# Kernel optimization log

Measured on AMD Instinct MI355X. Metric: run time of the kernel, lower is better.

The kernel has to match this reference:

```python
import jax, jax.numpy as jnp
import numpy as np

B, P, N, E, H, KD, M = 64, 100, 1000, 512, 8, 64, 10
SQRT_E = float(np.sqrt(E))
CLIP = 10.0


def _heads(x):
    # [b, n, H*KD] -> [b, H, n, KD]
    b, n, _ = x.shape
    return x.reshape(b, n, H, KD).transpose(0, 2, 1, 3)


def setup_inputs() -> dict:
    key = jax.random.key(0)
    ks = jax.random.split(key, 20)
    f = jnp.float32
    s = 0.02  # weight init scale
    return {
        "encoded_last_node": jax.random.normal(ks[0], (B, P, E), f),
        "encoded_last_agents": jax.random.normal(ks[1], (B, P, E), f),
        "cur_dist": jax.random.uniform(ks[2], (B, P, N), f, 1e-3, 1.0),
        "ninf_mask": jnp.zeros((B, P, N), f),
        "lengths": jax.random.uniform(ks[3], (B, P, M), f),
        "max_dis": jax.random.uniform(ks[4], (B, P, 1), f),
        "remain_max_dis": jax.random.uniform(ks[5], (B, P, 1), f),
        "q_first": 0.5 * jax.random.normal(ks[6], (B, H, P, KD), f),
        "k": 0.5 * jax.random.normal(ks[7], (B, H, N, KD), f),
        "v": 0.5 * jax.random.normal(ks[8], (B, H, N, KD), f),
        "single_head_key": 0.5 * jax.random.normal(ks[9], (B, E, N), f),
        "Wq_last_w": s * jax.random.normal(ks[10], (H * KD, 2 * E + 2), f),
        "dis_emb_w": s * jax.random.normal(ks[11], (H * KD, 4), f),
        "mh_w": s * jax.random.normal(ks[12], (E, H * KD), f),
        "mh_b": s * jax.random.normal(ks[13], (E,), f),
        "dist_alpha": jnp.ones((1,), f),
        "depot_num": jax.random.randint(ks[14], (B,), 1, M + 1),
        "route_cnt": jax.random.randint(ks[15], (B, P, 1), 0, M),
        "left_city": jax.random.randint(ks[16], (B, P), 0, N + 1),
        "city_num": N,
    }


def reference(encoded_last_node, encoded_last_agents, cur_dist, ninf_mask,
              lengths, max_dis, remain_max_dis, q_first, k, v, single_head_key,
              Wq_last_w, dis_emb_w, mh_w, mh_b, dist_alpha,
              depot_num, route_cnt, left_city, city_num):
    # route_num = depot_num - 1, broadcast to route_cnt shape [B,P,1]
    route_num = jnp.broadcast_to(depot_num[:, None, None], route_cnt.shape) - 1
    g_cur = jnp.take_along_axis(lengths, route_cnt, axis=-1)    # [B,P,1]
    g_route = jnp.take_along_axis(lengths, route_num, axis=-1)  # [B,P,1]
    q_info_in = jnp.concatenate([g_cur, g_route, max_dis, remain_max_dis], axis=-1)  # [B,P,4]
    q_info = _heads(q_info_in @ dis_emb_w.T)  # [B,H,P,KD]

    frac = 1.0 - (route_cnt + 1).astype(jnp.float32) / (route_num + 1).astype(jnp.float32)
    lc = left_city[:, :, None].astype(jnp.float32) / city_num
    q_last_in = jnp.concatenate([encoded_last_node, encoded_last_agents, frac, lc], axis=-1)  # [B,P,2E+2]
    q_last = _heads(q_last_in @ Wq_last_w.T)  # [B,H,P,KD]

    q = q_first + q_last + q_info  # [B,H,P,KD]

    # masked multi-head attention (rank3 ninf mask)
    score = jnp.einsum("bhpd,bhnd->bhpn", q, k) / jnp.sqrt(jnp.float32(KD))
    score = score + ninf_mask[:, None, :, :]
    w = jax.nn.softmax(score, axis=-1)
    out = jnp.einsum("bhpn,bhnd->bhpd", w, v)
    out_concat = out.transpose(0, 2, 1, 3).reshape(out.shape[0], out.shape[2], H * KD)  # [B,P,H*KD]
    mh = out_concat @ mh_w.T + mh_b  # [B,P,E]

    # single-head distance-biased scoring
    score2 = jnp.einsum("bpe,ben->bpn", mh, single_head_key)  # [B,P,N]
    max_dist = jnp.max(cur_dist, axis=-1, keepdims=True)
    cur_dist_out = -cur_dist / max_dist
    score_clipped = CLIP * jnp.tanh(score2 / SQRT_E + dist_alpha * cur_dist_out)
    probs = jax.nn.softmax(score_clipped + ninf_mask, axis=-1)
    return probs
```

## Files before the change

### kernel.cpp

```cpp
#include <hip/hip_runtime.h>
#include <hip/hip_bf16.h>

#define BB 64
#define PP 100
#define NN 1000
#define EE 512
#define HH 8
#define KDD 64
#define MM 10
#define ROWS (BB*PP)
#define K1K 1026
#define INVSQE 0.044194173824159216f
#define CLIPV 10.0f

union F4 { float4 v; float f[4]; };

using bf16x8 = __attribute__((ext_vector_type(8))) short;
using f32x4  = __attribute__((ext_vector_type(4))) float;

__device__ inline unsigned short f2bf(float x) {
  unsigned u = __float_as_uint(x);
  u += 0x7FFFu + ((u >> 16) & 1u);
  return (unsigned short)(u >> 16);
}

__device__ inline float fast_tanh(float x) {
  float e = __expf(2.0f * x);
  return 1.0f - 2.0f / (e + 1.0f);
}

__global__ __launch_bounds__(256) void k_rowmax(const float* __restrict__ cd,
                                                float* __restrict__ rmax) {
  int row = blockIdx.x * 4 + (threadIdx.x >> 6);
  int lane = threadIdx.x & 63;
  const float* src = cd + (size_t)row * NN;
  float m = -1e30f;
  for (int i = lane; i < NN; i += 64) m = fmaxf(m, src[i]);
  #pragma unroll
  for (int off = 32; off; off >>= 1) m = fmaxf(m, __shfl_xor(m, off));
  if (lane == 0) rmax[row] = m;
}

__global__ __launch_bounds__(256) void k_qgemm(
    const float* __restrict__ eln, const float* __restrict__ ela,
    const float* __restrict__ lengths, const float* __restrict__ max_dis,
    const float* __restrict__ remain, const float* __restrict__ q_first,
    const float* __restrict__ Wq, const float* __restrict__ dis_emb,
    const int* __restrict__ depot, const int* __restrict__ route_cnt,
    const int* __restrict__ left_city, const int* __restrict__ city_num,
    float* __restrict__ qout) {
  __shared__ unsigned short Xs[64][40];
  __shared__ unsigned short Ws[64][40];
  __shared__ float info_s[64][4];
  __shared__ float fl_s[64][2];
  const int t = threadIdx.x;
  const int lane = t & 63;
  const int w = t >> 6;
  const int lr = lane & 15, lg = lane >> 4;
  const int rowBase = blockIdx.y * 64, colBase = blockIdx.x * 64;

  if (t < 64) {
    int row = rowBase + t;
    int b = row / PP;
    int rc = route_cnt[row];
    int rn = depot[b] - 1;
    info_s[t][0] = lengths[row * MM + rc];
    info_s[t][1] = lengths[row * MM + rn];
    info_s[t][2] = max_dis[row];
    info_s[t][3] = remain[row];
    fl_s[t][0] = 1.0f - (float)(rc + 1) / (float)(rn + 1);
    fl_s[t][1] = (float)left_city[row] / (float)city_num[0];
  }

  f32x4 acc[4];
  #pragma unroll
  for (int m = 0; m < 4; ++m) { acc[m][0] = 0.f; acc[m][1] = 0.f; acc[m][2] = 0.f; acc[m][3] = 0.f; }

  for (int kt = 0; kt < 32; ++kt) {
    const float* xsrc = (kt < 16) ? eln : ela;
    const int koff = (kt & 15) * 32;
    __syncthreads();
    #pragma unroll
    for (int i = 0; i < 2; ++i) {
      int s = i * 256 + t;
      int r = s >> 3, c4 = (s & 7) * 4;
      F4 xv, wv;
      xv.v = *(const float4*)&xsrc[(size_t)(rowBase + r) * 512 + koff + c4];
      wv.v = *(const float4*)&Wq[(size_t)(colBase + r) * K1K + kt * 32 + c4];
      unsigned short* xd = &Xs[r][c4];
      unsigned short* wd = &Ws[r][c4];
      xd[0] = f2bf(xv.f[0]); xd[1] = f2bf(xv.f[1]); xd[2] = f2bf(xv.f[2]); xd[3] = f2bf(xv.f[3]);
      wd[0] = f2bf(wv.f[0]); wd[1] = f2bf(wv.f[1]); wd[2] = f2bf(wv.f[2]); wd[3] = f2bf(wv.f[3]);
    }
    __syncthreads();
    bf16x8 bfr = *(bf16x8*)&Ws[w * 16 + lr][lg * 8];
    #pragma unroll
    for (int m = 0; m < 4; ++m) {
      bf16x8 af = *(bf16x8*)&Xs[m * 16 + lr][lg * 8];
      acc[m] = __builtin_amdgcn_mfma_f32_16x16x32_bf16(af, bfr, acc[m], 0, 0, 0);
    }
  }

  const int o = colBase + w * 16 + lr;
  F4 de; de.v = *(const float4*)&dis_emb[(size_t)o * 4];
  const float wq1024 = Wq[(size_t)o * K1K + 1024];
  const float wq1025 = Wq[(size_t)o * K1K + 1025];
  const int h = o >> 6, kd = o & 63;
  #pragma unroll
  for (int m = 0; m < 4; ++m) {
    #pragma unroll
    for (int j = 0; j < 4; ++j) {
      int r = m * 16 + lg * 4 + j;
      int row = rowBase + r;
      int b = row / PP, p = row % PP;
      F4 inf; inf.v = *(const float4*)&info_s[r][0];
      float v = acc[m][j]
              + inf.f[0] * de.f[0] + inf.f[1] * de.f[1]
              + inf.f[2] * de.f[2] + inf.f[3] * de.f[3]
              + fl_s[r][0] * wq1024 + fl_s[r][1] * wq1025
              + q_first[(((size_t)b * HH + h) * PP + p) * KDD + kd];
      qout[(size_t)row * 512 + o] = v;
    }
  }
}

__global__ __launch_bounds__(256) void k_attn(
    const float* __restrict__ qin, const float* __restrict__ kk,
    const float* __restrict__ vv, const float* __restrict__ mask,
    float* __restrict__ attn_out) {
  __shared__ unsigned short Kl[64][72];
  __shared__ unsigned short Vt[64][72];
  __shared__ float PM[112][68];

  const int t = threadIdx.x;
  const int lane = t & 63;
  const int w = t >> 6;
  const int lr = lane & 15;
  const int lg = lane >> 4;
  const int bh = blockIdx.x, b = bh >> 3, h = bh & 7;

  #pragma unroll
  for (int i = 0; i < 7; ++i) {
    int idx = i * 256 + t;
    int r = idx >> 4, c4 = (idx & 15) * 4;
    float4 qv = make_float4(0.f, 0.f, 0.f, 0.f);
    if (r < PP)
      qv = *(const float4*)&qin[((size_t)(b * PP + r)) * 512 + h * 64 + c4];
    qv.x *= 0.125f; qv.y *= 0.125f; qv.z *= 0.125f; qv.w *= 0.125f;
    *(float4*)&PM[r][c4] = qv;
  }
  __syncthreads();

  bf16x8 qf[2][2];
  #pragma unroll
  for (int u = 0; u < 2; ++u) {
    int tt = w + 4 * u;
    if (tt < 7) {
      #pragma unroll
      for (int kb = 0; kb < 2; ++kb) {
        F4 p0, p1;
        p0.v = *(const float4*)&PM[tt * 16 + lr][kb * 32 + lg * 8];
        p1.v = *(const float4*)&PM[tt * 16 + lr][kb * 32 + lg * 8 + 4];
        bf16x8 f;
        #pragma unroll
        for (int i = 0; i < 4; ++i) { f[i] = (short)f2bf(p0.f[i]); f[i + 4] = (short)f2bf(p1.f[i]); }
        qf[u][kb] = f;
      }
    }
  }
  __syncthreads();

  float Mx[2][4], Lx[2][4];
  f32x4 Oa[2][4];
  #pragma unroll
  for (int u = 0; u < 2; ++u)
    #pragma unroll
    for (int j = 0; j < 4; ++j) {
      Mx[u][j] = -1e30f; Lx[u][j] = 0.f;
      Oa[u][j][0] = 0.f; Oa[u][j][1] = 0.f; Oa[u][j][2] = 0.f; Oa[u][j][3] = 0.f;
    }

  for (int ch = 0; ch < 16; ++ch) {
    const int n0 = ch * 64;
    #pragma unroll
    for (int i = 0; i < 4; ++i) {
      int idx = i * 256 + t;
      int r = idx >> 4, c4 = (idx & 15) * 4;
      int n = n0 + r;
      F4 kv; kv.v = make_float4(0.f, 0.f, 0.f, 0.f);
      if (n < NN) kv.v = *(const float4*)&kk[(((size_t)bh * NN) + n) * 64 + c4];
      Kl[r][c4 + 0] = f2bf(kv.f[0]); Kl[r][c4 + 1] = f2bf(kv.f[1]);
      Kl[r][c4 + 2] = f2bf(kv.f[2]); Kl[r][c4 + 3] = f2bf(kv.f[3]);
    }
    {
      int a = t >> 4, b2 = t & 15;
      F4 rowv[4];
      #pragma unroll
      for (int r = 0; r < 4; ++r) {
        int n = n0 + 4 * a + r;
        rowv[r].v = (n < NN) ? *(const float4*)&vv[(((size_t)bh * NN) + n) * 64 + 4 * b2]
                             : make_float4(0.f, 0.f, 0.f, 0.f);
      }
      #pragma unroll
      for (int c = 0; c < 4; ++c) {
        unsigned short* dst = &Vt[4 * b2 + c][4 * a];
        dst[0] = f2bf(rowv[0].f[c]); dst[1] = f2bf(rowv[1].f[c]);
        dst[2] = f2bf(rowv[2].f[c]); dst[3] = f2bf(rowv[3].f[c]);
      }
    }
    #pragma unroll
    for (int i = 0; i < 7; ++i) {
      int idx = i * 256 + t;
      int r = idx >> 4, c4 = (idx & 15) * 4;
      int n = n0 + c4;
      F4 mv; mv.v = make_float4(0.f, 0.f, 0.f, 0.f);
      if (r < PP) {
        if (n + 3 < NN) {
          mv.v = *(const float4*)&mask[((size_t)(b * PP + r)) * NN + n];
        } else {
          #pragma unroll
          for (int j = 0; j < 4; ++j)
            mv.f[j] = (n + j < NN) ? mask[((size_t)(b * PP + r)) * NN + n + j] : -1e30f;
        }
      }
      *(float4*)&PM[r][c4] = mv.v;
    }
    __syncthreads();

    float rsv[2][4];
    #pragma unroll
    for (int u = 0; u < 2; ++u) {
      int tt = w + 4 * u;
      if (tt >= 7) continue;
      f32x4 sa[4];
      #pragma unroll
      for (int nb = 0; nb < 4; ++nb) { sa[nb][0] = 0.f; sa[nb][1] = 0.f; sa[nb][2] = 0.f; sa[nb][3] = 0.f; }
      #pragma unroll
      for (int kb = 0; kb < 2; ++kb)
        #pragma unroll
        for (int nb = 0; nb < 4; ++nb) {
          bf16x8 kf = *(bf16x8*)&Kl[nb * 16 + lr][kb * 32 + lg * 8];
          sa[nb] = __builtin_amdgcn_mfma_f32_16x16x32_bf16(qf[u][kb], kf, sa[nb], 0, 0, 0);
        }
      #pragma unroll
      for (int j = 0; j < 4; ++j) {
        int pl = tt * 16 + lg * 4 + j;
        float s0 = sa[0][j] + PM[pl][lr];
        float s1 = sa[1][j] + PM[pl][16 + lr];
        float s2 = sa[2][j] + PM[pl][32 + lr];
        float s3 = sa[3][j] + PM[pl][48 + lr];
        float cm = fmaxf(fmaxf(s0, s1), fmaxf(s2, s3));
        #pragma unroll
        for (int off = 1; off < 16; off <<= 1) cm = fmaxf(cm, __shfl_xor(cm, off));
        float Mn = fmaxf(Mx[u][j], cm);
        float r = __expf(Mx[u][j] - Mn);
        float e0 = __expf(s0 - Mn), e1 = __expf(s1 - Mn);
        float e2 = __expf(s2 - Mn), e3 = __expf(s3 - Mn);
        float sum = (e0 + e1) + (e2 + e3);
        #pragma unroll
        for (int off = 1; off < 16; off <<= 1) sum += __shfl_xor(sum, off);
        Lx[u][j] = Lx[u][j] * r + sum;
        Mx[u][j] = Mn;
        rsv[u][j] = r;
        PM[pl][lr] = e0; PM[pl][16 + lr] = e1; PM[pl][32 + lr] = e2; PM[pl][48 + lr] = e3;
      }
    }
    __syncthreads();

    #pragma unroll
    for (int u = 0; u < 2; ++u) {
      int tt = w + 4 * u;
      if (tt >= 7) continue;
      #pragma unroll
      for (int dt = 0; dt < 4; ++dt) {
        f32x4 o = Oa[u][dt];
        o[0] *= rsv[u][0]; o[1] *= rsv[u][1]; o[2] *= rsv[u][2]; o[3] *= rsv[u][3];
        Oa[u][dt] = o;
      }
      #pragma unroll
      for (int kb = 0; kb < 2; ++kb) {
        F4 p0, p1;
        p0.v = *(const float4*)&PM[tt * 16 + lr][kb * 32 + lg * 8];
        p1.v = *(const float4*)&PM[tt * 16 + lr][kb * 32 + lg * 8 + 4];
        bf16x8 pf;
        #pragma unroll
        for (int i = 0; i < 4; ++i) { pf[i] = (short)f2bf(p0.f[i]); pf[i + 4] = (short)f2bf(p1.f[i]); }
        #pragma unroll
        for (int dt = 0; dt < 4; ++dt) {
          bf16x8 vf = *(bf16x8*)&Vt[dt * 16 + lr][kb * 32 + lg * 8];
          Oa[u][dt] = __builtin_amdgcn_mfma_f32_16x16x32_bf16(pf, vf, Oa[u][dt], 0, 0, 0);
        }
      }
    }
    __syncthreads();
  }

  #pragma unroll
  for (int u = 0; u < 2; ++u) {
    int tt = w + 4 * u;
    if (tt >= 7) continue;
    #pragma unroll
    for (int j = 0; j < 4; ++j) {
      int p = tt * 16 + lg * 4 + j;
      if (p >= PP) continue;
      float L = Lx[u][j];
      float inv = (L > 0.f) ? 1.0f / L : 0.f;
      #pragma unroll
      for (int dt = 0; dt < 4; ++dt)
        attn_out[((size_t)(b * PP + p)) * 512 + h * 64 + dt * 16 + lr] = Oa[u][dt][j] * inv;
    }
  }
}

__global__ __launch_bounds__(256) void k_mhgemm(
    const float* __restrict__ A, const float* __restrict__ W,
    const float* __restrict__ bias, float* __restrict__ out) {
  __shared__ unsigned short Xs[64][40];
  __shared__ unsigned short Ws[64][40];
  const int t = threadIdx.x;
  const int lane = t & 63;
  const int w = t >> 6;
  const int lr = lane & 15, lg = lane >> 4;
  const int rowBase = blockIdx.y * 64, colBase = blockIdx.x * 64;

  f32x4 acc[4];
  #pragma unroll
  for (int m = 0; m < 4; ++m) { acc[m][0] = 0.f; acc[m][1] = 0.f; acc[m][2] = 0.f; acc[m][3] = 0.f; }

  for (int kt = 0; kt < 16; ++kt) {
    const int koff = kt * 32;
    __syncthreads();
    #pragma unroll
    for (int i = 0; i < 2; ++i) {
      int s = i * 256 + t;
      int r = s >> 3, c4 = (s & 7) * 4;
      F4 xv, wv;
      xv.v = *(const float4*)&A[(size_t)(rowBase + r) * 512 + koff + c4];
      wv.v = *(const float4*)&W[(size_t)(colBase + r) * 512 + koff + c4];
      unsigned short* xd = &Xs[r][c4];
      unsigned short* wd = &Ws[r][c4];
      xd[0] = f2bf(xv.f[0]); xd[1] = f2bf(xv.f[1]); xd[2] = f2bf(xv.f[2]); xd[3] = f2bf(xv.f[3]);
      wd[0] = f2bf(wv.f[0]); wd[1] = f2bf(wv.f[1]); wd[2] = f2bf(wv.f[2]); wd[3] = f2bf(wv.f[3]);
    }
    __syncthreads();
    bf16x8 bfr = *(bf16x8*)&Ws[w * 16 + lr][lg * 8];
    #pragma unroll
    for (int m = 0; m < 4; ++m) {
      bf16x8 af = *(bf16x8*)&Xs[m * 16 + lr][lg * 8];
      acc[m] = __builtin_amdgcn_mfma_f32_16x16x32_bf16(af, bfr, acc[m], 0, 0, 0);
    }
  }

  const int o = colBase + w * 16 + lr;
  const float bv = bias[o];
  #pragma unroll
  for (int m = 0; m < 4; ++m) {
    #pragma unroll
    for (int j = 0; j < 4; ++j) {
      int row = rowBase + m * 16 + lg * 4 + j;
      out[(size_t)row * 512 + o] = acc[m][j] + bv;
    }
  }
}

__global__ __launch_bounds__(256) void k_final_score(
    const float* __restrict__ mh, const float* __restrict__ shk,
    const float* __restrict__ cur_dist, const float* __restrict__ rmax,
    const float* __restrict__ mask, const float* __restrict__ dist_alpha,
    float* __restrict__ sc_out) {
  __shared__ unsigned short As[112][40];
  __shared__ unsigned short Bt[64][40];
  const int t = threadIdx.x;
  const int lane = t & 63;
  const int w = t >> 6;
  const int lr = lane & 15, lg = lane >> 4;
  const int n0 = blockIdx.x * 64, b = blockIdx.y;

  f32x4 acc[7];
  #pragma unroll
  for (int m = 0; m < 7; ++m) { acc[m][0] = 0.f; acc[m][1] = 0.f; acc[m][2] = 0.f; acc[m][3] = 0.f; }

  for (int kt = 0; kt < 16; ++kt) {
    const int k0 = kt * 32;
    __syncthreads();
    #pragma unroll
    for (int i = 0; i < 4; ++i) {
      int s = i * 256 + t;
      if (s < 896) {
        int r = s >> 3, c4 = (s & 7) * 4;
        F4 xv; xv.v = make_float4(0.f, 0.f, 0.f, 0.f);
        if (r < PP) xv.v = *(const float4*)&mh[(size_t)(b * PP + r) * 512 + k0 + c4];
        unsigned short* xd = &As[r][c4];
        xd[0] = f2bf(xv.f[0]); xd[1] = f2bf(xv.f[1]); xd[2] = f2bf(xv.f[2]); xd[3] = f2bf(xv.f[3]);
      }
    }
    if (t < 128) {
      int a = t & 15, kb = t >> 4;
      F4 rowv[4];
      #pragma unroll
      for (int r = 0; r < 4; ++r) {
        int k = k0 + 4 * kb + r;
        int n = n0 + 4 * a;
        rowv[r].v = (n < NN) ? *(const float4*)&shk[((size_t)b * EE + k) * NN + n]
                             : make_float4(0.f, 0.f, 0.f, 0.f);
      }
      #pragma unroll
      for (int c = 0; c < 4; ++c) {
        unsigned short* dst = &Bt[4 * a + c][4 * kb];
        dst[0] = f2bf(rowv[0].f[c]); dst[1] = f2bf(rowv[1].f[c]);
        dst[2] = f2bf(rowv[2].f[c]); dst[3] = f2bf(rowv[3].f[c]);
      }
    }
    __syncthreads();
    bf16x8 bfr = *(bf16x8*)&Bt[w * 16 + lr][lg * 8];
    #pragma unroll
    for (int m = 0; m < 7; ++m) {
      bf16x8 af = *(bf16x8*)&As[m * 16 + lr][lg * 8];
      acc[m] = __builtin_amdgcn_mfma_f32_16x16x32_bf16(af, bfr, acc[m], 0, 0, 0);
    }
  }

  const float alpha = dist_alpha[0];
  const int n = n0 + w * 16 + lr;
  if (n < NN) {
    #pragma unroll
    for (int m = 0; m < 7; ++m) {
      #pragma unroll
      for (int j = 0; j < 4; ++j) {
        int p = m * 16 + lg * 4 + j;
        if (p >= PP) continue;
        size_t rb = (size_t)(b * PP + p) * NN;
        float rmx = rmax[b * PP + p];
        float cd = cur_dist[rb + n];
        float mk = mask[rb + n];
        sc_out[rb + n] = CLIPV * fast_tanh(acc[m][j] * INVSQE - alpha * cd / rmx) + mk;
      }
    }
  }
}

__global__ __launch_bounds__(256) void k_softmax(const float* __restrict__ sc,
                                                 float* __restrict__ out) {
  __shared__ float redm[4];
  __shared__ float redsum[4];
  const int row = blockIdx.x;
  const int t = threadIdx.x;
  const float* src = sc + (size_t)row * NN;
  float v0[4];
  float m = -1e30f;
  #pragma unroll
  for (int i = 0; i < 4; ++i) {
    int n = i * 256 + t;
    v0[i] = (n < NN) ? src[n] : -1e30f;
    m = fmaxf(m, v0[i]);
  }
  #pragma unroll
  for (int off = 32; off; off >>= 1) m = fmaxf(m, __shfl_xor(m, off));
  int wid = t >> 6, lane = t & 63;
  if (lane == 0) redm[wid] = m;
  __syncthreads();
  m = fmaxf(fmaxf(redm[0], redm[1]), fmaxf(redm[2], redm[3]));
  float e[4];
  float s = 0.f;
  #pragma unroll
  for (int i = 0; i < 4; ++i) {
    int n = i * 256 + t;
    e[i] = (n < NN) ? __expf(v0[i] - m) : 0.f;
    s += e[i];
  }
  #pragma unroll
  for (int off = 32; off; off >>= 1) s += __shfl_xor(s, off);
  if (lane == 0) redsum[wid] = s;
  __syncthreads();
  s = redsum[0] + redsum[1] + redsum[2] + redsum[3];
  float inv = 1.0f / s;
  #pragma unroll
  for (int i = 0; i < 4; ++i) {
    int n = i * 256 + t;
    if (n < NN) out[(size_t)row * NN + n] = e[i] * inv;
  }
}

extern "C" void kernel_launch(void* const* d_in, const int* in_sizes, int n_in,
                              void* d_out, int out_size, void* d_ws, size_t ws_size,
                              hipStream_t stream) {
  const float* eln       = (const float*)d_in[0];
  const float* ela       = (const float*)d_in[1];
  const float* cur_dist  = (const float*)d_in[2];
  const float* ninf      = (const float*)d_in[3];
  const float* lengths   = (const float*)d_in[4];
  const float* max_dis   = (const float*)d_in[5];
  const float* remain    = (const float*)d_in[6];
  const float* q_first   = (const float*)d_in[7];
  const float* kten      = (const float*)d_in[8];
  const float* vten      = (const float*)d_in[9];
  const float* shk       = (const float*)d_in[10];
  const float* Wq        = (const float*)d_in[11];
  const float* dis_emb   = (const float*)d_in[12];
  const float* mh_w      = (const float*)d_in[13];
  const float* mh_b      = (const float*)d_in[14];
  const float* dalpha    = (const float*)d_in[15];
  const int*   depot     = (const int*)d_in[16];
  const int*   route_cnt = (const int*)d_in[17];
  const int*   left_city = (const int*)d_in[18];
  const int*   city_num  = (const int*)d_in[19];
  float* out = (float*)d_out;

  float* ws      = (float*)d_ws;
  float* q_ws    = ws;
  float* attn_ws = q_ws + (size_t)ROWS * 512;
  float* mh_ws   = attn_ws + (size_t)ROWS * 512;
  float* sc_ws   = mh_ws + (size_t)ROWS * 512;
  float* rmax_ws = sc_ws + (size_t)ROWS * NN;

  k_rowmax<<<ROWS / 4, 256, 0, stream>>>(cur_dist, rmax_ws);
  k_qgemm<<<dim3(8, 100), 256, 0, stream>>>(eln, ela, lengths, max_dis, remain,
                                            q_first, Wq, dis_emb, depot, route_cnt,
                                            left_city, city_num, q_ws);
  k_attn<<<BB * HH, 256, 0, stream>>>(q_ws, kten, vten, ninf, attn_ws);
  k_mhgemm<<<dim3(8, 100), 256, 0, stream>>>(attn_ws, mh_w, mh_b, mh_ws);
  k_final_score<<<dim3(16, 64), 256, 0, stream>>>(mh_ws, shk, cur_dist, rmax_ws,
                                                  ninf, dalpha, sc_ws);
  k_softmax<<<ROWS, 256, 0, stream>>>(sc_ws, out);
}
```

Baseline: 320.2 us.

## Split attention over key dimension into four partitions with merge kernel

Replaces the single attention kernel (512 blocks, one per batch-head) with a split-K flash-decoding style scheme. Four blocks per batch-head each handle 256 keys and write bf16 partial outputs plus the running max and sum. A separate merge kernel then rescales and combines them. This raises grid parallelism on a GPU with many CUs, at the cost of an extra launch, partial-result traffic through global memory, and bf16 rounding of the unnormalized partial outputs. The V-transpose load indexing is also swapped, which changes the global read coalescing pattern.

Result: slower. 352.6 us (+10.1%).

```diff
diff --git a/kernel.cpp b/kernel.cpp
--- a/kernel.cpp
+++ b/kernel.cpp
@@ -12,6 +12,7 @@
 #define K1K 1026
 #define INVSQE 0.044194173824159216f
 #define CLIPV 10.0f
+#define NPART 4
 
 union F4 { float4 v; float f[4]; };
 
@@ -22,6 +23,10 @@
   unsigned u = __float_as_uint(x);
   u += 0x7FFFu + ((u >> 16) & 1u);
   return (unsigned short)(u >> 16);
+}
+
+__device__ inline float bf2f(unsigned short s) {
+  return __uint_as_float(((unsigned)s) << 16);
 }
 
 __device__ inline float fast_tanh(float x) {
@@ -124,10 +129,11 @@
   }
 }
 
-__global__ __launch_bounds__(256) void k_attn(
+__global__ __launch_bounds__(256) void k_attn_part(
     const float* __restrict__ qin, const float* __restrict__ kk,
     const float* __restrict__ vv, const float* __restrict__ mask,
-    float* __restrict__ attn_out) {
+    unsigned short* __restrict__ pO, float* __restrict__ pm,
+    float* __restrict__ pl) {
   __shared__ unsigned short Kl[64][72];
   __shared__ unsigned short Vt[64][72];
   __shared__ float PM[112][68];
@@ -137,7 +143,12 @@
   const int w = t >> 6;
   const int lr = lane & 15;
   const int lg = lane >> 4;
-  const int bh = blockIdx.x, b = bh >> 3, h = bh & 7;
+  const int gid = blockIdx.x;
+  const int b = gid & 63;
+  const int X = gid >> 6;
+  const int h = X & 7, part = X >> 3;
+  const int bh = b * HH + h;
+  const int nbase = part * 256;
 
   #pragma unroll
   for (int i = 0; i < 7; ++i) {
@@ -180,8 +191,8 @@
       Oa[u][j][0] = 0.f; Oa[u][j][1] = 0.f; Oa[u][j][2] = 0.f; Oa[u][j][3] = 0.f;
     }
 
-  for (int ch = 0; ch < 16; ++ch) {
-    const int n0 = ch * 64;
+  for (int ch = 0; ch < 4; ++ch) {
+    const int n0 = nbase + ch * 64;
     #pragma unroll
     for (int i = 0; i < 4; ++i) {
       int idx = i * 256 + t;
@@ -193,17 +204,17 @@
       Kl[r][c4 + 2] = f2bf(kv.f[2]); Kl[r][c4 + 3] = f2bf(kv.f[3]);
     }
     {
-      int a = t >> 4, b2 = t & 15;
+      int b2 = t & 15, a = t >> 4;
       F4 rowv[4];
       #pragma unroll
       for (int r = 0; r < 4; ++r) {
-        int n = n0 + 4 * a + r;
-        rowv[r].v = (n < NN) ? *(const float4*)&vv[(((size_t)bh * NN) + n) * 64 + 4 * b2]
+        int n = n0 + 4 * b2 + r;
+        rowv[r].v = (n < NN) ? *(const float4*)&vv[(((size_t)bh * NN) + n) * 64 + 4 * a]
                              : make_float4(0.f, 0.f, 0.f, 0.f);
       }
       #pragma unroll
       for (int c = 0; c < 4; ++c) {
-        unsigned short* dst = &Vt[4 * b2 + c][4 * a];
+        unsigned short* dst = &Vt[4 * a + c][4 * b2];
         dst[0] = f2bf(rowv[0].f[c]); dst[1] = f2bf(rowv[1].f[c]);
         dst[2] = f2bf(rowv[2].f[c]); dst[3] = f2bf(rowv[3].f[c]);
       }
@@ -244,11 +255,11 @@
         }
       #pragma unroll
       for (int j = 0; j < 4; ++j) {
-        int pl = tt * 16 + lg * 4 + j;
-        float s0 = sa[0][j] + PM[pl][lr];
-        float s1 = sa[1][j] + PM[pl][16 + lr];
-        float s2 = sa[2][j] + PM[pl][32 + lr];
-        float s3 = sa[3][j] + PM[pl][48 + lr];
+        int plidx = tt * 16 + lg * 4 + j;
+        float s0 = sa[0][j] + PM[plidx][lr];
+        float s1 = sa[1][j] + PM[plidx][16 + lr];
+        float s2 = sa[2][j] + PM[plidx][32 + lr];
+        float s3 = sa[3][j] + PM[plidx][48 + lr];
         float cm = fmaxf(fmaxf(s0, s1), fmaxf(s2, s3));
         #pragma unroll
         for (int off = 1; off < 16; off <<= 1) cm = fmaxf(cm, __shfl_xor(cm, off));
@@ -262,7 +273,7 @@
         Lx[u][j] = Lx[u][j] * r + sum;
         Mx[u][j] = Mn;
         rsv[u][j] = r;
-        PM[pl][lr] = e0; PM[pl][16 + lr] = e1; PM[pl][32 + lr] = e2; PM[pl][48 + lr] = e3;
+        PM[plidx][lr] = e0; PM[plidx][16 + lr] = e1; PM[plidx][32 + lr] = e2; PM[plidx][48 + lr] = e3;
       }
     }
     __syncthreads();
@@ -303,13 +314,44 @@
     for (int j = 0; j < 4; ++j) {
       int p = tt * 16 + lg * 4 + j;
       if (p >= PP) continue;
-      float L = Lx[u][j];
-      float inv = (L > 0.f) ? 1.0f / L : 0.f;
       #pragma unroll
       for (int dt = 0; dt < 4; ++dt)
-        attn_out[((size_t)(b * PP + p)) * 512 + h * 64 + dt * 16 + lr] = Oa[u][dt][j] * inv;
-    }
-  }
+        pO[(size_t)gid * (PP * 64) + p * 64 + dt * 16 + lr] = f2bf(Oa[u][dt][j]);
+      if (lr == 0) {
+        pm[gid * PP + p] = Mx[u][j];
+        pl[gid * PP + p] = Lx[u][j];
+      }
+    }
+  }
+}
+
+__global__ __launch_bounds__(256) void k_attn_merge(
+    const unsigned short* __restrict__ pO, const float* __restrict__ pm,
+    const float* __restrict__ pl, float* __restrict__ attn_out) {
+  const int rid = blockIdx.x * 4 + (threadIdx.x >> 6);
+  const int d = threadIdx.x & 63;
+  const int b = rid / (HH * PP);
+  const int rem = rid % (HH * PP);
+  const int h = rem / PP, p = rem % PP;
+  float m[NPART], l[NPART];
+  float M = -1e30f;
+  #pragma unroll
+  for (int q = 0; q < NPART; ++q) {
+    int slot = (q * 8 + h) * 64 + b;
+    m[q] = pm[slot * PP + p];
+    l[q] = pl[slot * PP + p];
+    M = fmaxf(M, m[q]);
+  }
+  float L = 0.f, O = 0.f;
+  #pragma unroll
+  for (int q = 0; q < NPART; ++q) {
+    int slot = (q * 8 + h) * 64 + b;
+    float sc = __expf(m[q] - M);
+    L += l[q] * sc;
+    O += bf2f(pO[(size_t)slot * (PP * 64) + p * 64 + d]) * sc;
+  }
+  float inv = (L > 0.f) ? 1.0f / L : 0.f;
+  attn_out[((size_t)(b * PP + p)) * 512 + h * 64 + d] = O * inv;
 }
 
 __global__ __launch_bounds__(256) void k_mhgemm(
@@ -513,11 +555,17 @@
   float* sc_ws   = mh_ws + (size_t)ROWS * 512;
   float* rmax_ws = sc_ws + (size_t)ROWS * NN;
 
+  unsigned short* pO_ws = (unsigned short*)mh_ws;
+  float* pm_ws = mh_ws + (size_t)6553600;
+  float* pl_ws = pm_ws + (size_t)2048 * PP;
+
   k_rowmax<<<ROWS / 4, 256, 0, stream>>>(cur_dist, rmax_ws);
   k_qgemm<<<dim3(8, 100), 256, 0, stream>>>(eln, ela, lengths, max_dis, remain,
                                             q_first, Wq, dis_emb, depot, route_cnt,
                                             left_city, city_num, q_ws);
-  k_attn<<<BB * HH, 256, 0, stream>>>(q_ws, kten, vten, ninf, attn_ws);
+  k_attn_part<<<BB * HH * NPART, 256, 0, stream>>>(q_ws, kten, vten, ninf,
+                                                   pO_ws, pm_ws, pl_ws);
+  k_attn_merge<<<(ROWS * HH) / 4, 256, 0, stream>>>(pO_ws, pm_ws, pl_ws, attn_ws);
   k_mhgemm<<<dim3(8, 100), 256, 0, stream>>>(attn_ws, mh_w, mh_b, mh_ws);
   k_final_score<<<dim3(16, 64), 256, 0, stream>>>(mh_ws, shk, cur_dist, rmax_ws,
                                                   ninf, dalpha, sc_ws);
```
